# Optimization experiments

Measured on AMD Instinct MI355X. Metric: run time of the kernel, lower is better.

Reference implementation:

```python
import jax, jax.numpy as jnp
import numpy as np

L, H, HM, E = 2, 1024, 256, 64  # layers, hidden, hyper hidden, hyper embedding
B, T, D = 64, 256, 1024         # batch, time, input size (D == H so layers stack)


def setup_inputs() -> dict:
    key = jax.random.key(0)
    ks = jax.random.split(key, 16)
    n = jax.random.normal
    inp = {
        'x':   n(ks[0], (B, T, D), jnp.float32),
        # main LSTM weights: 4 gates (i,f,g,o); last dim is the input dim
        'Wx':  n(ks[1], (L, 4, H, D), jnp.float32) / np.sqrt(D),
        'Wh':  n(ks[2], (L, 4, H, H), jnp.float32) / np.sqrt(H),
        # hyper (meta) LSTM: input is concat(x_t, h) of size D+H
        'Wmx': n(ks[3], (L, 4 * HM, D + H), jnp.float32) / np.sqrt(D + H),
        'Wmh': n(ks[4], (L, 4 * HM, HM), jnp.float32) / np.sqrt(HM),
        'bm':  jnp.zeros((L, 4 * HM), jnp.float32),
        # hyper embeddings z per gate (hidden->4xE projections)
        'Wzx': n(ks[5], (L, HM, 4, E), jnp.float32) / np.sqrt(HM),
        'bzx': jnp.ones((L, 4, E), jnp.float32),
        'Wzh': n(ks[6], (L, HM, 4, E), jnp.float32) / np.sqrt(HM),
        'bzh': jnp.ones((L, 4, E), jnp.float32),
        'Wzb': n(ks[7], (L, HM, 4, E), jnp.float32) / np.sqrt(HM),
        # embedding -> per-unit modulation (E->H per gate)
        'Px':  n(ks[8], (L, 4, E, H), jnp.float32) / np.sqrt(E),
        'Ph':  n(ks[9], (L, 4, E, H), jnp.float32) / np.sqrt(E),
        'Pb':  n(ks[10], (L, 4, E, H), jnp.float32) / np.sqrt(E),
    }
    return inp


def _meta_lstm_forward(x, Wx, Wh, Wmx, Wmh, bm, Wzx, bzx, Wzh, bzh, Wzb, Px, Ph, Pb):
    Bb = x.shape[0]
    inp = x
    for l in range(L):
        def step(carry, xt, l=l):
            h, c, mh, mc = carry
            # hyper LSTM step on concat(x_t, h)
            xcat = jnp.concatenate([xt, h], axis=-1)
            mpre = xcat @ Wmx[l].T + mh @ Wmh[l].T + bm[l]
            mi, mf, mg, mo = jnp.split(mpre, 4, axis=-1)
            mc2 = jax.nn.sigmoid(mf) * mc + jax.nn.sigmoid(mi) * jnp.tanh(mg)
            mh2 = jax.nn.sigmoid(mo) * jnp.tanh(mc2)
            # gate embeddings and per-unit modulation vectors [B,4,H]
            zx = jnp.einsum('bm,mge->bge', mh2, Wzx[l]) + bzx[l]
            zh = jnp.einsum('bm,mge->bge', mh2, Wzh[l]) + bzh[l]
            zb = jnp.einsum('bm,mge->bge', mh2, Wzb[l])
            dx = jnp.einsum('bge,geh->bgh', zx, Px[l])
            dh = jnp.einsum('bge,geh->bgh', zh, Ph[l])
            db = jnp.einsum('bge,geh->bgh', zb, Pb[l])
            # main LSTM gate pre-activations, hyper-modulated
            gx = jnp.einsum('bd,ghd->bgh', xt, Wx[l])
            gh = jnp.einsum('bk,ghk->bgh', h, Wh[l])
            pre = dx * gx + dh * gh + db
            i_, f_, g_, o_ = pre[:, 0], pre[:, 1], pre[:, 2], pre[:, 3]
            c2 = jax.nn.sigmoid(f_) * c + jax.nn.sigmoid(i_) * jnp.tanh(g_)
            h2 = jax.nn.sigmoid(o_) * jnp.tanh(c2)
            return (h2, c2, mh2, mc2), h2
        init = (jnp.zeros((Bb, H), x.dtype), jnp.zeros((Bb, H), x.dtype),
                jnp.zeros((Bb, HM), x.dtype), jnp.zeros((Bb, HM), x.dtype))
        xs = jnp.swapaxes(inp, 0, 1)  # [T,B,D]
        _, hs = jax.lax.scan(step, init, xs)
        inp = jnp.swapaxes(hs, 0, 1)  # [B,T,H]
    return inp


def reference(x, Wx, Wh, Wmx, Wmh, bm, Wzx, bzx, Wzh, bzh, Wzb, Px, Ph, Pb):
    return _meta_lstm_forward(x, Wx, Wh, Wmx, Wmh, bm, Wzx, bzx, Wzh, bzh, Wzb, Px, Ph, Pb)
```

## Files before the change

kernel.cpp:

```cpp
#include <hip/hip_runtime.h>
#include <hip/hip_cooperative_groups.h>

namespace cg = cooperative_groups;

#define Bb 64
#define Tt 256
#define Dd 1024
#define Hh 1024
#define HMm 256
#define Ee 64

__device__ __forceinline__ float b2f(unsigned short u){
    union{unsigned int i; float f;} v; v.i = ((unsigned int)u) << 16; return v.f;
}
__device__ __forceinline__ unsigned short f2bf(float f){
    union{float f; unsigned int i;} v; v.f = f;
    unsigned int x = v.i;
    unsigned int r = (x + 0x7fffu + ((x >> 16) & 1u)) >> 16;
    return (unsigned short)r;
}
__device__ __forceinline__ void up2(unsigned int u, float& lo, float& hi){
    union{unsigned int i; float f;} x, y;
    x.i = u << 16; y.i = u & 0xffff0000u; lo = x.f; hi = y.f;
}
__device__ __forceinline__ float sigf(float x){ return 1.f/(1.f + expf(-x)); }

__device__ __forceinline__ float ldT(const unsigned short* p){ return b2f(*p); }
__device__ __forceinline__ float ldT(const float* p){ return *p; }
__device__ __forceinline__ void stT(unsigned short* p, float v){ *p = f2bf(v); }
__device__ __forceinline__ void stT(float* p, float v){ *p = v; }

__device__ __forceinline__ void ld8(const unsigned short* p, float* f){
    uint4 u = *(const uint4*)(const void*)p;
    up2(u.x,f[0],f[1]); up2(u.y,f[2],f[3]); up2(u.z,f[4],f[5]); up2(u.w,f[6],f[7]);
}
__device__ __forceinline__ void ld8(const float* p, float* f){
    float4 a = *(const float4*)(const void*)p;
    float4 b = *(const float4*)(const void*)(p+4);
    f[0]=a.x; f[1]=a.y; f[2]=a.z; f[3]=a.w; f[4]=b.x; f[5]=b.y; f[6]=b.z; f[7]=b.w;
}
__device__ __forceinline__ float dot8(const float* a, const float* b, float acc){
    #pragma unroll
    for(int i=0;i<8;i++) acc += a[i]*b[i];
    return acc;
}

__global__ void k_detect(const unsigned short* __restrict__ x, int* __restrict__ flag){
    int tid = threadIdx.x;
    float v = fabsf(b2f(x[2 * tid]));
    bool in = (v > 1e-4f) && (v < 50.f);
    unsigned long long m = __ballot(in);
    if(tid == 0) *flag = (__popcll(m) >= 32) ? 0 : 1;
}

__global__ __launch_bounds__(1024, 4) void coop_rnn_bf16(
    const unsigned short* x,
    const unsigned short* __restrict__ Wx, const unsigned short* __restrict__ Wh,
    const unsigned short* __restrict__ Wmx, const unsigned short* __restrict__ Wmh,
    const unsigned short* __restrict__ bm,
    const unsigned short* __restrict__ Wzx, const unsigned short* __restrict__ bzx,
    const unsigned short* __restrict__ Wzh, const unsigned short* __restrict__ bzh,
    const unsigned short* __restrict__ Wzb,
    const unsigned short* __restrict__ Px, const unsigned short* __restrict__ Ph,
    const unsigned short* __restrict__ Pb,
    unsigned short* out, float* ws, const int* flag)
{
    if(*flag != 0) return;
    cg::grid_group grid = cg::this_grid();

    float* h0   = ws;
    float* h1   = ws + 65536;
    float* cst  = ws + 131072;
    float* m0   = ws + 196608;
    float* m1   = ws + 212992;
    float* mcst = ws + 229376;
    float* z    = ws + 245760;
    unsigned short* xbuf16 = (unsigned short*)(ws + 294912);

    int tid = threadIdx.x, bid = blockIdx.x;

    __shared__ __align__(16) unsigned short sWx[16][4][264];
    __shared__ __align__(16) unsigned short sWh[16][4][264];
    __shared__ __align__(16) unsigned short sWmxX[4][4][264];
    __shared__ __align__(16) unsigned short sWmxH[4][4][264];
    __shared__ __align__(16) unsigned short sWmh[4][4][72];
    __shared__ __align__(16) unsigned short sWz[3][4][72];
    __shared__ __align__(16) unsigned short sP[3][4][64][4];
    __shared__ float sBm[4], sBz[2];
    __shared__ float sA[256];
    __shared__ float spre[1024];

    for(int l = 0; l < 2; l++){
        const unsigned short* xseq = l ? out : x;
        const unsigned short* Wx_l  = Wx  + (size_t)l * 4194304;
        const unsigned short* Wh_l  = Wh  + (size_t)l * 4194304;
        const unsigned short* Wmx_l = Wmx + (size_t)l * 2097152;
        const unsigned short* Wmh_l = Wmh + (size_t)l * 262144;
        const unsigned short* bm_l  = bm  + l * 1024;
        const unsigned short* Wz0 = Wzx + l * 65536;
        const unsigned short* Wz1 = Wzh + l * 65536;
        const unsigned short* Wz2 = Wzb + l * 65536;
        const unsigned short* bz0 = bzx + l * 256;
        const unsigned short* bz1 = bzh + l * 256;
        const unsigned short* Px_l = Px + l * 262144;
        const unsigned short* Ph_l = Ph + l * 262144;
        const unsigned short* Pb_l = Pb + l * 262144;

        {
            int gid = bid * 1024 + tid;
            if(gid < 65536){ h0[gid] = 0.f; cst[gid] = 0.f; }
            if(gid < 16384){ m0[gid] = 0.f; mcst[gid] = 0.f; }
        }

        for(int idx = tid; idx < 16384; idx += 1024){
            int rr = idx >> 10, k = idx & 1023;
            int g = rr >> 2, hh = rr & 3;
            size_t n = (size_t)(g * 1024 + bid * 4 + hh);
            sWx[rr][k >> 8][k & 255] = Wx_l[n * 1024 + k];
        }
        for(int idx = tid; idx < 16384; idx += 1024){
            int rr = idx >> 10, k = idx & 1023;
            int g = rr >> 2, hh = rr & 3;
            size_t n = (size_t)(g * 1024 + bid * 4 + hh);
            sWh[rr][k >> 8][k & 255] = Wh_l[n * 1024 + k];
        }
        for(int idx = tid; idx < 4096; idx += 1024){
            int r = idx >> 10, k = idx & 1023;
            size_t row = (size_t)(r * 256 + bid);
            sWmxX[r][k >> 8][k & 255] = Wmx_l[row * 2048 + k];
            sWmxH[r][k >> 8][k & 255] = Wmx_l[row * 2048 + 1024 + k];
        }
        {
            int r = tid >> 8, m = tid & 255;
            sWmh[r][m >> 6][m & 63] = Wmh_l[(size_t)(r * 256 + bid) * 256 + m];
        }
        if(tid < 768){
            int s_ = tid >> 8, m = tid & 255;
            const unsigned short* W = (s_ == 0) ? Wz0 : ((s_ == 1) ? Wz1 : Wz2);
            sWz[s_][m >> 6][m & 63] = W[m * 256 + bid];
        }
        {
            int g = tid >> 8, e = (tid >> 2) & 63, hh = tid & 3;
            int pi = (g * 64 + e) * 1024 + bid * 4 + hh;
            sP[0][g][e][hh] = Px_l[pi];
            sP[1][g][e][hh] = Ph_l[pi];
            sP[2][g][e][hh] = Pb_l[pi];
        }
        if(tid < 4) sBm[tid] = ldT(&bm_l[tid * 256 + bid]);
        if(tid == 4) sBz[0] = ldT(&bz0[bid]);
        if(tid == 5) sBz[1] = ldT(&bz1[bid]);

        float *hp = h0, *hn = h1, *mp = m0, *mn = m1;
        grid.sync();

        for(int t = 0; t < 256; t++){
            {
                int sg = bid * 1024 + tid;
                if(sg < 65536){
                    int xb = sg >> 10, xd = sg & 1023;
                    xbuf16[sg] = xseq[((size_t)xb * Tt + t) * Dd + xd];
                }

                int r  = tid >> 8;
                int b  = (tid >> 2) & 63;
                int ks = tid & 3;
                const unsigned short* wxp = &sWmxX[r][ks][0];
                const unsigned short* whp_ = &sWmxH[r][ks][0];
                const unsigned short* wmp = &sWmh[r][ks][0];
                const unsigned short* xr = xseq + ((size_t)b * Tt + t) * Dd + ks * 256;
                const float* hr = hp + b * 1024 + ks * 256;
                const float* mr = mp + b * 256 + ks * 64;
                float a0 = 0.f, a1 = 0.f, a2 = 0.f, a3 = 0.f;
                float wf[8], vf[8];
                for(int k = 0; k < 256; k += 16){
                    ld8(wxp + k, wf);     ld8(xr + k, vf);     a0 = dot8(wf, vf, a0);
                    ld8(wxp + k + 8, wf); ld8(xr + k + 8, vf); a1 = dot8(wf, vf, a1);
                }
                for(int k = 0; k < 256; k += 16){
                    ld8(whp_ + k, wf);     ld8(hr + k, vf);     a2 = dot8(wf, vf, a2);
                    ld8(whp_ + k + 8, wf); ld8(hr + k + 8, vf); a3 = dot8(wf, vf, a3);
                }
                for(int m = 0; m < 64; m += 16){
                    ld8(wmp + m, wf);     ld8(mr + m, vf);     a0 = dot8(wf, vf, a0);
                    ld8(wmp + m + 8, wf); ld8(mr + m + 8, vf); a1 = dot8(wf, vf, a1);
                }
                float a = (a0 + a1) + (a2 + a3);
                a += __shfl_xor(a, 1);
                a += __shfl_xor(a, 2);
                if(ks == 0) sA[r * 64 + b] = a + sBm[r];
            }
            __syncthreads();
            if(tid < 64){
                int b = tid;
                float mi = sA[b], mf = sA[64 + b], mg = sA[128 + b], mo = sA[192 + b];
                int idx = b * 256 + bid;
                float mc2 = sigf(mf) * mcst[idx] + sigf(mi) * tanhf(mg);
                mcst[idx] = mc2;
                mn[idx] = sigf(mo) * tanhf(mc2);
            }
            grid.sync();

            if(tid < 768){
                int s_ = tid >> 8, sub = tid & 255;
                int b = sub >> 2, ks = sub & 3;
                const unsigned short* wz = &sWz[s_][ks][0];
                const float* mr = mn + b * 256 + ks * 64;
                float acc = 0.f; float wf[8], vf[8];
                for(int m = 0; m < 64; m += 16){
                    ld8(wz + m, wf);     ld8(mr + m, vf);     acc = dot8(wf, vf, acc);
                    ld8(wz + m + 8, wf); ld8(mr + m + 8, vf); acc = dot8(wf, vf, acc);
                }
                acc += __shfl_xor(acc, 1);
                acc += __shfl_xor(acc, 2);
                if(ks == 0){
                    float biasv = (s_ == 0) ? sBz[0] : ((s_ == 1) ? sBz[1] : 0.f);
                    z[((s_ * 256) + bid) * 64 + b] = acc + biasv;
                }
            }
            grid.sync();

            {
                int r16 = tid >> 6;
                int g = r16 >> 2, hh = r16 & 3;
                int bg = (tid >> 2) & 15;
                int ks = tid & 3;
                int b0 = bg * 4;
                const unsigned short* wxr = &sWx[r16][ks][0];
                const unsigned short* whr = &sWh[r16][ks][0];
                float gx[4] = {0,0,0,0}, gh[4] = {0,0,0,0};
                for(int k = 0; k < 256; k += 8){
                    float wf[8]; ld8(wxr + k, wf);
                    #pragma unroll
                    for(int i = 0; i < 4; i++){
                        float xf[8]; ld8(xbuf16 + (b0 + i) * 1024 + ks * 256 + k, xf);
                        gx[i] = dot8(wf, xf, gx[i]);
                    }
                }
                for(int k = 0; k < 256; k += 8){
                    float wf[8]; ld8(whr + k, wf);
                    #pragma unroll
                    for(int i = 0; i < 4; i++){
                        float hf[8]; ld8(hp + (b0 + i) * 1024 + ks * 256 + k, hf);
                        gh[i] = dot8(wf, hf, gh[i]);
                    }
                }
                float dx[4] = {0,0,0,0}, dh[4] = {0,0,0,0}, db[4] = {0,0,0,0};
                int e0 = ks * 16;
                for(int e = e0; e < e0 + 16; e++){
                    int zc = g * 64 + e;
                    float pxv = b2f(sP[0][g][e][hh]);
                    float phv = b2f(sP[1][g][e][hh]);
                    float pbv = b2f(sP[2][g][e][hh]);
                    const float4 zx4 = *(const float4*)&z[(0 * 256 + zc) * 64 + b0];
                    const float4 zh4 = *(const float4*)&z[(1 * 256 + zc) * 64 + b0];
                    const float4 zb4 = *(const float4*)&z[(2 * 256 + zc) * 64 + b0];
                    dx[0] += zx4.x * pxv; dx[1] += zx4.y * pxv; dx[2] += zx4.z * pxv; dx[3] += zx4.w * pxv;
                    dh[0] += zh4.x * phv; dh[1] += zh4.y * phv; dh[2] += zh4.z * phv; dh[3] += zh4.w * phv;
                    db[0] += zb4.x * pbv; db[1] += zb4.y * pbv; db[2] += zb4.z * pbv; db[3] += zb4.w * pbv;
                }
                #pragma unroll
                for(int i = 0; i < 4; i++){
                    gx[i] += __shfl_xor(gx[i], 1); gx[i] += __shfl_xor(gx[i], 2);
                    gh[i] += __shfl_xor(gh[i], 1); gh[i] += __shfl_xor(gh[i], 2);
                    dx[i] += __shfl_xor(dx[i], 1); dx[i] += __shfl_xor(dx[i], 2);
                    dh[i] += __shfl_xor(dh[i], 1); dh[i] += __shfl_xor(dh[i], 2);
                    db[i] += __shfl_xor(db[i], 1); db[i] += __shfl_xor(db[i], 2);
                }
                if(ks == 0){
                    #pragma unroll
                    for(int i = 0; i < 4; i++)
                        spre[r16 * 64 + b0 + i] = dx[i] * gx[i] + dh[i] * gh[i] + db[i];
                }
            }
            __syncthreads();
            if(tid < 256){
                int hh = tid >> 6, b = tid & 63;
                float pi_ = spre[(0 * 4 + hh) * 64 + b];
                float pf_ = spre[(1 * 4 + hh) * 64 + b];
                float pg_ = spre[(2 * 4 + hh) * 64 + b];
                float po_ = spre[(3 * 4 + hh) * 64 + b];
                int h = bid * 4 + hh;
                int idx = b * 1024 + h;
                float c2 = sigf(pf_) * cst[idx] + sigf(pi_) * tanhf(pg_);
                float h2 = sigf(po_) * tanhf(c2);
                cst[idx] = c2;
                hn[idx] = h2;
                stT(&out[((size_t)b * Tt + t) * Dd + h], h2);
            }
            grid.sync();

            float* tp = hp; hp = hn; hn = tp;
            tp = mp; mp = mn; mn = tp;
        }
    }
}

__global__ __launch_bounds__(1024, 4) void coop_rnn_f32(
    const float* x,
    const float* __restrict__ Wx, const float* __restrict__ Wh,
    const float* __restrict__ Wmx, const float* __restrict__ Wmh, const float* __restrict__ bm,
    const float* __restrict__ Wzx, const float* __restrict__ bzx,
    const float* __restrict__ Wzh, const float* __restrict__ bzh, const float* __restrict__ Wzb,
    const float* __restrict__ Px, const float* __restrict__ Ph, const float* __restrict__ Pb,
    float* out, float* ws, const int* flag)
{
    if(*flag != 1) return;
    cg::grid_group grid = cg::this_grid();

    float* h0   = ws;
    float* h1   = ws + 65536;
    float* cst  = ws + 131072;
    float* m0   = ws + 196608;
    float* m1   = ws + 212992;
    float* mcst = ws + 229376;
    float* z    = ws + 245760;
    float* xbuf = ws + 294912;

    int tid = threadIdx.x, bid = blockIdx.x;

    __shared__ float sA[256];
    __shared__ float spre[1024];

    for(int l = 0; l < 2; l++){
        const float* xseq = l ? out : x;
        const float* Wx_l  = Wx  + (size_t)l * 4194304;
        const float* Wh_l  = Wh  + (size_t)l * 4194304;
        const float* Wmx_l = Wmx + (size_t)l * 2097152;
        const float* Wmh_l = Wmh + (size_t)l * 262144;
        const float* bm_l  = bm  + l * 1024;
        const float* Wz0 = Wzx + l * 65536;
        const float* Wz1 = Wzh + l * 65536;
        const float* Wz2 = Wzb + l * 65536;
        const float* bz0 = bzx + l * 256;
        const float* bz1 = bzh + l * 256;
        const float* Px_l = Px + l * 262144;
        const float* Ph_l = Ph + l * 262144;
        const float* Pb_l = Pb + l * 262144;

        {
            int gid = bid * 1024 + tid;
            if(gid < 65536){ h0[gid] = 0.f; cst[gid] = 0.f; }
            if(gid < 16384){ m0[gid] = 0.f; mcst[gid] = 0.f; }
        }
        float *hp = h0, *hn = h1, *mp = m0, *mn = m1;
        grid.sync();

        for(int t = 0; t < 256; t++){
            {
                int sg = bid * 1024 + tid;
                if(sg < 65536){
                    int xb = sg >> 10, xd = sg & 1023;
                    xbuf[sg] = ldT(&xseq[((size_t)xb * Tt + t) * Dd + xd]);
                }
                int r  = tid >> 8;
                int b  = (tid >> 2) & 63;
                int ks = tid & 3;
                int row = r * 256 + bid;
                const float* wr = Wmx_l + (size_t)row * 2048;
                const float* wm = Wmh_l + (size_t)row * 256;
                const float* xr = xseq + ((size_t)b * Tt + t) * Dd;
                const float* hr = hp + b * 1024;
                const float* mr = mp + b * 256;
                float a0 = 0.f, a1 = 0.f, a2 = 0.f, a3 = 0.f;
                float wf[8], vf[8];
                int k0 = ks * 256;
                for(int k = k0; k < k0 + 256; k += 16){
                    ld8(wr + k, wf);      ld8(xr + k, vf);      a0 = dot8(wf, vf, a0);
                    ld8(wr + k + 8, wf);  ld8(xr + k + 8, vf);  a1 = dot8(wf, vf, a1);
                }
                for(int k = k0; k < k0 + 256; k += 16){
                    ld8(wr + 1024 + k, wf);     ld8(hr + k, vf);     a2 = dot8(wf, vf, a2);
                    ld8(wr + 1024 + k + 8, wf); ld8(hr + k + 8, vf); a3 = dot8(wf, vf, a3);
                }
                int ms = ks * 64;
                for(int m = ms; m < ms + 64; m += 16){
                    ld8(wm + m, wf);     ld8(mr + m, vf);     a0 = dot8(wf, vf, a0);
                    ld8(wm + m + 8, wf); ld8(mr + m + 8, vf); a1 = dot8(wf, vf, a1);
                }
                float a = (a0 + a1) + (a2 + a3);
                a += __shfl_xor(a, 1);
                a += __shfl_xor(a, 2);
                if(ks == 0) sA[r * 64 + b] = a + ldT(&bm_l[row]);
            }
            __syncthreads();
            if(tid < 64){
                int b = tid;
                float mi = sA[b], mf = sA[64 + b], mg = sA[128 + b], mo = sA[192 + b];
                int idx = b * 256 + bid;
                float mc2 = sigf(mf) * mcst[idx] + sigf(mi) * tanhf(mg);
                mcst[idx] = mc2;
                mn[idx] = sigf(mo) * tanhf(mc2);
            }
            grid.sync();

            if(bid < 192){
                int s_ = bid >> 6, b = bid & 63;
                int ks = tid >> 8, col = tid & 255;
                const float* W = (s_ == 0) ? Wz0 : ((s_ == 1) ? Wz1 : Wz2);
                const float* mr = mn + b * 256;
                float acc = 0.f;
                int ms = ks * 64;
                #pragma unroll 8
                for(int m = ms; m < ms + 64; m++)
                    acc += mr[m] * ldT(&W[m * 256 + col]);
                spre[tid] = acc;
                __syncthreads();
                if(tid < 256){
                    float biasv = (s_ == 0) ? ldT(&bz0[tid]) : ((s_ == 1) ? ldT(&bz1[tid]) : 0.f);
                    z[(s_ * 64 + b) * 256 + tid] =
                        biasv + ((spre[tid] + spre[256 + tid]) + (spre[512 + tid] + spre[768 + tid]));
                }
            }
            grid.sync();

            {
                int r16 = tid >> 6;
                int g = r16 >> 2, hh = r16 & 3;
                int bg = (tid >> 2) & 15;
                int ks = tid & 3;
                int h = bid * 4 + hh;
                int n = g * 1024 + h;
                int b0 = bg * 4;
                const float* wxr = Wx_l + (size_t)n * 1024;
                const float* whr = Wh_l + (size_t)n * 1024;
                float gx[4] = {0,0,0,0}, gh[4] = {0,0,0,0};
                int k0 = ks * 256;
                for(int k = k0; k < k0 + 256; k += 8){
                    float wf[8]; ld8(wxr + k, wf);
                    #pragma unroll
                    for(int i = 0; i < 4; i++){
                        float xf[8]; ld8(xbuf + (b0 + i) * 1024 + k, xf);
                        gx[i] = dot8(wf, xf, gx[i]);
                    }
                }
                for(int k = k0; k < k0 + 256; k += 8){
                    float wf[8]; ld8(whr + k, wf);
                    #pragma unroll
                    for(int i = 0; i < 4; i++){
                        float hf[8]; ld8(hp + (b0 + i) * 1024 + k, hf);
                        gh[i] = dot8(wf, hf, gh[i]);
                    }
                }
                float dx[4] = {0,0,0,0}, dh[4] = {0,0,0,0}, db[4] = {0,0,0,0};
                int e0 = ks * 16;
                for(int e = e0; e < e0 + 16; e++){
                    int pi = (g * 64 + e) * 1024 + h;
                    float pxv = ldT(&Px_l[pi]);
                    float phv = ldT(&Ph_l[pi]);
                    float pbv = ldT(&Pb_l[pi]);
                    int zc = g * 64 + e;
                    #pragma unroll
                    for(int i = 0; i < 4; i++){
                        int b = b0 + i;
                        dx[i] += z[(b) * 256 + zc] * pxv;
                        dh[i] += z[(64 + b) * 256 + zc] * phv;
                        db[i] += z[(128 + b) * 256 + zc] * pbv;
                    }
                }
                #pragma unroll
                for(int i = 0; i < 4; i++){
                    gx[i] += __shfl_xor(gx[i], 1); gx[i] += __shfl_xor(gx[i], 2);
                    gh[i] += __shfl_xor(gh[i], 1); gh[i] += __shfl_xor(gh[i], 2);
                    dx[i] += __shfl_xor(dx[i], 1); dx[i] += __shfl_xor(dx[i], 2);
                    dh[i] += __shfl_xor(dh[i], 1); dh[i] += __shfl_xor(dh[i], 2);
                    db[i] += __shfl_xor(db[i], 1); db[i] += __shfl_xor(db[i], 2);
                }
                if(ks == 0){
                    #pragma unroll
                    for(int i = 0; i < 4; i++)
                        spre[r16 * 64 + b0 + i] = dx[i] * gx[i] + dh[i] * gh[i] + db[i];
                }
            }
            __syncthreads();
            if(tid < 256){
                int hh = tid >> 6, b = tid & 63;
                float pi_ = spre[(0 * 4 + hh) * 64 + b];
                float pf_ = spre[(1 * 4 + hh) * 64 + b];
                float pg_ = spre[(2 * 4 + hh) * 64 + b];
                float po_ = spre[(3 * 4 + hh) * 64 + b];
                int h = bid * 4 + hh;
                int idx = b * 1024 + h;
                float c2 = sigf(pf_) * cst[idx] + sigf(pi_) * tanhf(pg_);
                float h2 = sigf(po_) * tanhf(c2);
                cst[idx] = c2;
                hn[idx] = h2;
                stT(&out[((size_t)b * Tt + t) * Dd + h], h2);
            }
            grid.sync();

            float* tp = hp; hp = hn; hn = tp;
            tp = mp; mp = mn; mn = tp;
        }
    }
}

static void launch_bf16(void* const* d_in, void* d_out, float* ws, int* flag, hipStream_t stream){
    const unsigned short* xp   = (const unsigned short*)d_in[0];
    const unsigned short* Wxp  = (const unsigned short*)d_in[1];
    const unsigned short* Whp  = (const unsigned short*)d_in[2];
    const unsigned short* Wmxp = (const unsigned short*)d_in[3];
    const unsigned short* Wmhp = (const unsigned short*)d_in[4];
    const unsigned short* bmp  = (const unsigned short*)d_in[5];
    const unsigned short* Wzxp = (const unsigned short*)d_in[6];
    const unsigned short* bzxp = (const unsigned short*)d_in[7];
    const unsigned short* Wzhp = (const unsigned short*)d_in[8];
    const unsigned short* bzhp = (const unsigned short*)d_in[9];
    const unsigned short* Wzbp = (const unsigned short*)d_in[10];
    const unsigned short* Pxp  = (const unsigned short*)d_in[11];
    const unsigned short* Php  = (const unsigned short*)d_in[12];
    const unsigned short* Pbp  = (const unsigned short*)d_in[13];
    unsigned short* outp = (unsigned short*)d_out;
    void* args[] = {
        (void*)&xp, (void*)&Wxp, (void*)&Whp, (void*)&Wmxp, (void*)&Wmhp, (void*)&bmp,
        (void*)&Wzxp, (void*)&bzxp, (void*)&Wzhp, (void*)&bzhp, (void*)&Wzbp,
        (void*)&Pxp, (void*)&Php, (void*)&Pbp, (void*)&outp, (void*)&ws, (void*)&flag
    };
    hipLaunchCooperativeKernel((void*)coop_rnn_bf16, dim3(256), dim3(1024), args, 0, stream);
}

static void launch_f32(void* const* d_in, void* d_out, float* ws, int* flag, hipStream_t stream){
    const float* xp   = (const float*)d_in[0];
    const float* Wxp  = (const float*)d_in[1];
    const float* Whp  = (const float*)d_in[2];
    const float* Wmxp = (const float*)d_in[3];
    const float* Wmhp = (const float*)d_in[4];
    const float* bmp  = (const float*)d_in[5];
    const float* Wzxp = (const float*)d_in[6];
    const float* bzxp = (const float*)d_in[7];
    const float* Wzhp = (const float*)d_in[8];
    const float* bzhp = (const float*)d_in[9];
    const float* Wzbp = (const float*)d_in[10];
    const float* Pxp  = (const float*)d_in[11];
    const float* Php  = (const float*)d_in[12];
    const float* Pbp  = (const float*)d_in[13];
    float* outp = (float*)d_out;
    void* args[] = {
        (void*)&xp, (void*)&Wxp, (void*)&Whp, (void*)&Wmxp, (void*)&Wmhp, (void*)&bmp,
        (void*)&Wzxp, (void*)&bzxp, (void*)&Wzhp, (void*)&bzhp, (void*)&Wzbp,
        (void*)&Pxp, (void*)&Php, (void*)&Pbp, (void*)&outp, (void*)&ws, (void*)&flag
    };
    hipLaunchCooperativeKernel((void*)coop_rnn_f32, dim3(256), dim3(1024), args, 0, stream);
}

extern "C" void kernel_launch(void* const* d_in, const int* in_sizes, int n_in,
                              void* d_out, int out_size, void* d_ws, size_t ws_size,
                              hipStream_t stream) {
    (void)in_sizes; (void)n_in; (void)out_size; (void)ws_size;
    float* ws = (float*)d_ws;
    int* flag = (int*)(ws + 360448);

    k_detect<<<1, 64, 0, stream>>>((const unsigned short*)d_in[0], flag);
    launch_bf16(d_in, d_out, ws, flag, stream);
    launch_f32(d_in, d_out, ws, flag, stream);
}
```

Measured before the change: 287.7 ms.

## Keep per-block Wx/Wh rows and P slices resident in LDS across timesteps

At the start of each layer, every block copies its 16 rows of Wx and Wh and its slices of Px/Ph/Pb into padded shared-memory arrays. The per-timestep gate matvecs and modulation loops then read weights from LDS instead of global memory. The goal is to stop re-streaming about 32MB of main-LSTM weights from L2/HBM on all 256 recurrent steps. In exchange the block needs roughly 150KB of LDS, close to the per-CU limit, which could reduce occupancy or fail to launch on hardware with less LDS.

Result: faster. 252.8 ms (-12.1%).

```diff
diff --git a/kernel.cpp b/kernel.cpp
--- a/kernel.cpp
+++ b/kernel.cpp
@@ -318,6 +318,9 @@
 
     int tid = threadIdx.x, bid = blockIdx.x;
 
+    __shared__ __align__(16) float sWx[16][4][264];
+    __shared__ __align__(16) float sWh[16][4][264];
+    __shared__ __align__(16) float sP[3][4][64][5];
     __shared__ float sA[256];
     __shared__ float spre[1024];
 
@@ -342,6 +345,22 @@
             if(gid < 65536){ h0[gid] = 0.f; cst[gid] = 0.f; }
             if(gid < 16384){ m0[gid] = 0.f; mcst[gid] = 0.f; }
         }
+
+        for(int idx = tid; idx < 16384; idx += 1024){
+            int rr = idx >> 10, k = idx & 1023;
+            int g = rr >> 2, hh = rr & 3;
+            size_t n = (size_t)(g * 1024 + bid * 4 + hh);
+            sWx[rr][k >> 8][k & 255] = Wx_l[n * 1024 + k];
+            sWh[rr][k >> 8][k & 255] = Wh_l[n * 1024 + k];
+        }
+        {
+            int g = tid >> 8, e = (tid >> 2) & 63, hh = tid & 3;
+            int pi = (g * 64 + e) * 1024 + bid * 4 + hh;
+            sP[0][g][e][hh] = Px_l[pi];
+            sP[1][g][e][hh] = Ph_l[pi];
+            sP[2][g][e][hh] = Pb_l[pi];
+        }
+
         float *hp = h0, *hn = h1, *mp = m0, *mn = m1;
         grid.sync();
 
@@ -418,36 +437,32 @@
                 int g = r16 >> 2, hh = r16 & 3;
                 int bg = (tid >> 2) & 15;
                 int ks = tid & 3;
-                int h = bid * 4 + hh;
-                int n = g * 1024 + h;
                 int b0 = bg * 4;
-                const float* wxr = Wx_l + (size_t)n * 1024;
-                const float* whr = Wh_l + (size_t)n * 1024;
+                const float* wxr = &sWx[r16][ks][0];
+                const float* whr = &sWh[r16][ks][0];
                 float gx[4] = {0,0,0,0}, gh[4] = {0,0,0,0};
-                int k0 = ks * 256;
-                for(int k = k0; k < k0 + 256; k += 8){
+                for(int k = 0; k < 256; k += 8){
                     float wf[8]; ld8(wxr + k, wf);
                     #pragma unroll
                     for(int i = 0; i < 4; i++){
-                        float xf[8]; ld8(xbuf + (b0 + i) * 1024 + k, xf);
+                        float xf[8]; ld8(xbuf + (b0 + i) * 1024 + ks * 256 + k, xf);
                         gx[i] = dot8(wf, xf, gx[i]);
                     }
                 }
-                for(int k = k0; k < k0 + 256; k += 8){
+                for(int k = 0; k < 256; k += 8){
                     float wf[8]; ld8(whr + k, wf);
                     #pragma unroll
                     for(int i = 0; i < 4; i++){
-                        float hf[8]; ld8(hp + (b0 + i) * 1024 + k, hf);
+                        float hf[8]; ld8(hp + (b0 + i) * 1024 + ks * 256 + k, hf);
                         gh[i] = dot8(wf, hf, gh[i]);
                     }
                 }
                 float dx[4] = {0,0,0,0}, dh[4] = {0,0,0,0}, db[4] = {0,0,0,0};
                 int e0 = ks * 16;
                 for(int e = e0; e < e0 + 16; e++){
-                    int pi = (g * 64 + e) * 1024 + h;
-                    float pxv = ldT(&Px_l[pi]);
-                    float phv = ldT(&Ph_l[pi]);
-                    float pbv = ldT(&Pb_l[pi]);
+                    float pxv = sP[0][g][e][hh];
+                    float phv = sP[1][g][e][hh];
+                    float pbv = sP[2][g][e][hh];
                     int zc = g * 64 + e;
                     #pragma unroll
                     for(int i = 0; i < 4; i++){
```
